# Kernel optimization log

Measured on AMD Instinct MI355X. Metric: run time of the kernel, lower is better.

Reference implementation:

```python
import jax, jax.numpy as jnp
import numpy as np

DIM_CAP = 16   # capsule dim
NCLS = 17      # annotation_nr
BS = 16
T = 120        # chunk_size * fps
P = 22         # players per frame graph
G = BS * T     # number of graphs = 1920
N = G * P      # nodes = 42240
C_IN = 14
CHS = [16, 32, 64, 152]  # 8m,16m,32m,76m with m=2
BN_EPS = 1e-3


def _build_graph():
    # fully-connected directed edges within each 22-node graph (no self loops)
    ii, jj = np.meshgrid(np.arange(P), np.arange(P), indexing='ij')
    mask = ii != jj
    li, lj = ii[mask], jj[mask]               # (462,)
    base = (np.arange(G) * P)[:, None]
    src = (base + li[None, :]).reshape(-1)
    dst = (base + lj[None, :]).reshape(-1)
    edge_index = np.stack([src, dst]).astype(np.int64)   # (2, E)
    batch = np.repeat(np.arange(G), P).astype(np.int64)  # (N,)
    return jnp.asarray(edge_index), jnp.asarray(batch)


def setup_inputs() -> dict:
    key = jax.random.key(0)
    ks = jax.random.split(key, 16)
    edge_index, batch = _build_graph()
    E = edge_index.shape[1]
    x = jax.random.normal(ks[0], (N, C_IN), dtype=jnp.float32)
    edge_attr = jax.random.uniform(ks[1], (E, 5), dtype=jnp.float32)
    dims = [C_IN] + CHS
    params = {}
    for i in range(4):
        s = 1.0 / np.sqrt(dims[i])
        params[f'W{i+1}'] = jax.random.normal(ks[2 + i], (dims[i], dims[i + 1]), dtype=jnp.float32) * s
        params[f'b{i+1}'] = jnp.zeros((dims[i + 1],), dtype=jnp.float32)
    c_out = DIM_CAP * NCLS  # 272
    params['conv_w'] = jax.random.normal(ks[6], (c_out, CHS[-1], 3), dtype=jnp.float32) * (1.0 / np.sqrt(CHS[-1] * 3))
    params['conv_b'] = jnp.zeros((c_out,), dtype=jnp.float32)
    params['bn_gamma'] = jnp.ones((T,), dtype=jnp.float32)
    params['bn_beta'] = jnp.zeros((T,), dtype=jnp.float32)
    return dict(x=x, edge_index=edge_index, batch=batch, edge_attr=edge_attr, **params)


def _gcn_layer(x, src, dst, w_edge, W, b):
    # PyG GCNConv: x' = D^-1/2 (A + I) D^-1/2 (x W) + b, edge weights w, self-loop weight 1
    n = x.shape[0]
    h = x @ W
    loop = jnp.arange(n)
    src_f = jnp.concatenate([src, loop])
    dst_f = jnp.concatenate([dst, loop])
    w_f = jnp.concatenate([w_edge, jnp.ones((n,), h.dtype)])
    deg = jax.ops.segment_sum(w_f, dst_f, num_segments=n)
    dinv = jnp.where(deg > 0, jax.lax.rsqrt(deg), 0.0)
    norm = dinv[src_f] * w_f * dinv[dst_f]
    out = jax.ops.segment_sum(norm[:, None] * h[src_f], dst_f, num_segments=n)
    return out + b


def reference(x, edge_index, batch, edge_attr, W1, b1, W2, b2, W3, b3, W4, b4,
              conv_w, conv_b, bn_gamma, bn_beta):
    src, dst = edge_index[0], edge_index[1]
    ew = edge_attr[:, 4]
    h = jax.nn.relu(_gcn_layer(x, src, dst, ew, W1, b1))
    h = jax.nn.relu(_gcn_layer(h, src, dst, ew, W2, b2))
    h = jax.nn.relu(_gcn_layer(h, src, dst, ew, W3, b3))
    h = jax.nn.relu(_gcn_layer(h, src, dst, ew, W4, b4))
    # global mean pool per graph -> (G, 152)
    ones = jnp.ones((h.shape[0],), h.dtype)
    cnt = jax.ops.segment_sum(ones, batch, num_segments=G)
    pooled = jax.ops.segment_sum(h, batch, num_segments=G) / jnp.clip(cnt, 1.0)[:, None]
    # (BS, T, 152) -> (BS, 152, T); conv kernel (3,1) with pad (1,1) on T
    feat = pooled.reshape(BS, T, CHS[-1]).transpose(0, 2, 1)
    conv = jax.lax.conv_general_dilated(
        feat, conv_w, window_strides=(1,), padding=[(1, 1)],
        dimension_numbers=('NCH', 'OIH', 'NCH'))
    conv = conv + conv_b[None, :, None]            # (BS, 272, T)
    caps = conv.transpose(0, 2, 1).reshape(BS, T, DIM_CAP, NCLS)
    # BatchNorm2d(num_features=T) in eval mode: running mean 0, var 1
    scale = (bn_gamma / jnp.sqrt(1.0 + BN_EPS))[None, :, None, None]
    shift = bn_beta[None, :, None, None]
    s = jax.nn.sigmoid(caps * scale + shift)
    out = jnp.sqrt(jnp.sum(jnp.square(s - 0.5), axis=2) * 4.0 / DIM_CAP)
    return out  # (BS, T, NCLS)
```

## Files before the change

kernel.cpp:

```cpp
#include <hip/hip_runtime.h>

#define GROUPS 1920

__device__ __forceinline__ int rh(int r) { return (r + (r >> 3)) & 7; }
__device__ __forceinline__ int swz(int r, int c) {
    return (r << 5) + ((((c >> 2) ^ rh(r)) << 2) | (c & 3));
}
__device__ __forceinline__ int swz4(int r, int c4) {
    return (r << 5) + ((c4 ^ rh(r)) << 2);
}

template<int DIN, int KR>
__device__ __forceinline__ void layerA(const float* buf, float* Ut,
                                       const float* A, int tid)
{
    constexpr int NT = (DIN / KR) * 3;
    if (tid < NT) {
        const int kt = tid / 3, pt = tid - kt * 3;
        const int p0 = pt * 8;
        float acc[KR][8];
        #pragma unroll
        for (int j = 0; j < KR; ++j)
            #pragma unroll
            for (int a = 0; a < 8; ++a) acc[j][a] = 0.f;
        #pragma unroll 2
        for (int q = 0; q < 22; ++q) {
            const float4 a0 = *(const float4*)(A + q * 28 + p0);
            const float4 a1 = *(const float4*)(A + q * 28 + p0 + 4);
            float xv[KR];
            #pragma unroll
            for (int j = 0; j < KR; ++j) xv[j] = buf[swz(kt * KR + j, q)];
            #pragma unroll
            for (int j = 0; j < KR; ++j) {
                acc[j][0] = fmaf(xv[j], a0.x, acc[j][0]);
                acc[j][1] = fmaf(xv[j], a0.y, acc[j][1]);
                acc[j][2] = fmaf(xv[j], a0.z, acc[j][2]);
                acc[j][3] = fmaf(xv[j], a0.w, acc[j][3]);
                acc[j][4] = fmaf(xv[j], a1.x, acc[j][4]);
                acc[j][5] = fmaf(xv[j], a1.y, acc[j][5]);
                acc[j][6] = fmaf(xv[j], a1.z, acc[j][6]);
                acc[j][7] = fmaf(xv[j], a1.w, acc[j][7]);
            }
        }
        #pragma unroll
        for (int j = 0; j < KR; ++j) {
            const int k = kt * KR + j;
            *(float4*)(Ut + swz4(k, pt * 2)) =
                make_float4(acc[j][0], acc[j][1], acc[j][2], acc[j][3]);
            *(float4*)(Ut + swz4(k, pt * 2 + 1)) =
                make_float4(acc[j][4], acc[j][5], acc[j][6], acc[j][7]);
        }
    }
}

template<int DIN, int DOUT, int CR>
__device__ __forceinline__ void layerB(const float* __restrict__ W,
                                       const float* __restrict__ Bb,
                                       const float* Ut, float* buf, int tid)
{
    constexpr int NT = (DOUT / CR) * 3;
    if (tid < NT) {
        const int ct = tid / 3, pt = tid - ct * 3;
        const int c0 = ct * CR;
        float acc[CR][8];
        #pragma unroll
        for (int b = 0; b < CR; ++b) {
            const float bias = Bb[c0 + b];
            #pragma unroll
            for (int a = 0; a < 8; ++a) acc[b][a] = bias;
        }
        #pragma unroll 4
        for (int k = 0; k < DIN; ++k) {
            const float4 u0 = *(const float4*)(Ut + swz4(k, pt * 2));
            const float4 u1 = *(const float4*)(Ut + swz4(k, pt * 2 + 1));
            float wv[CR];
            if constexpr (CR == 1) {
                wv[0] = W[k * DOUT + c0];
            } else if constexpr (CR == 2) {
                const float2 w2 = *(const float2*)(W + k * DOUT + c0);
                wv[0] = w2.x; wv[1] = w2.y;
            } else {
                #pragma unroll
                for (int b = 0; b < CR; b += 4) {
                    const float4 w4 = *(const float4*)(W + k * DOUT + c0 + b);
                    wv[b] = w4.x; wv[b + 1] = w4.y; wv[b + 2] = w4.z; wv[b + 3] = w4.w;
                }
            }
            #pragma unroll
            for (int b = 0; b < CR; ++b) {
                acc[b][0] = fmaf(wv[b], u0.x, acc[b][0]);
                acc[b][1] = fmaf(wv[b], u0.y, acc[b][1]);
                acc[b][2] = fmaf(wv[b], u0.z, acc[b][2]);
                acc[b][3] = fmaf(wv[b], u0.w, acc[b][3]);
                acc[b][4] = fmaf(wv[b], u1.x, acc[b][4]);
                acc[b][5] = fmaf(wv[b], u1.y, acc[b][5]);
                acc[b][6] = fmaf(wv[b], u1.z, acc[b][6]);
                acc[b][7] = fmaf(wv[b], u1.w, acc[b][7]);
            }
        }
        #pragma unroll
        for (int b = 0; b < CR; ++b) {
            const int r = c0 + b;
            *(float4*)(buf + swz4(r, pt * 2)) =
                make_float4(fmaxf(acc[b][0], 0.f), fmaxf(acc[b][1], 0.f),
                            fmaxf(acc[b][2], 0.f), fmaxf(acc[b][3], 0.f));
            *(float4*)(buf + swz4(r, pt * 2 + 1)) =
                make_float4(fmaxf(acc[b][4], 0.f), fmaxf(acc[b][5], 0.f),
                            fmaxf(acc[b][6], 0.f), fmaxf(acc[b][7], 0.f));
        }
    }
}

__global__ __launch_bounds__(128, 4) void gcn_kernel(
    const float* __restrict__ x, const float* __restrict__ ea,
    const float* __restrict__ W1, const float* __restrict__ b1,
    const float* __restrict__ W2, const float* __restrict__ b2,
    const float* __restrict__ W3, const float* __restrict__ b3,
    const float* __restrict__ W4, const float* __restrict__ b4,
    float* __restrict__ pT)
{
    __shared__ __align__(16) float sA[24 * 28];
    __shared__ float dv[24];
    __shared__ __align__(16) float buf[64 * 32];
    __shared__ __align__(16) float Ut[64 * 32];

    const int tid = threadIdx.x;
    const int g = blockIdx.x;
    const int b = g / 120, t = g - b * 120;

    if (t == 0)
        for (int j = tid; j < 152 * 4; j += 128)
            pT[(((size_t)(b * 152) + (j >> 2)) << 7) + (j & 3)] = 0.f;
    if (t == 119)
        for (int j = tid; j < 152 * 4; j += 128)
            pT[(((size_t)(b * 152) + (j >> 2)) << 7) + 124 + (j & 3)] = 0.f;

    for (int idx = tid; idx < 24 * 28; idx += 128) {
        const int q = idx / 28, p = idx - q * 28;
        float v = 0.f;
        if (q < 22 && p < 22) {
            if (q == p) v = 1.0f;
            else {
                const int e = q * 21 + p - (p > q);
                v = ea[((size_t)g * 462 + e) * 5 + 4];
            }
        }
        sA[idx] = v;
    }
    for (int idx = tid; idx < 14 * 24; idx += 128) {
        const int k = idx / 24, p = idx - k * 24;
        buf[swz(k, p)] = (p < 22) ? x[((size_t)g * 22 + p) * 14 + k] : 0.f;
    }
    __syncthreads();

    if (tid < 24) {
        const int p = tid;
        float s = 0.f;
        #pragma unroll
        for (int q = 0; q < 22; ++q) s += sA[q * 28 + p];
        dv[p] = (s > 0.f) ? rsqrtf(s) : 0.f;
    }
    __syncthreads();
    for (int idx = tid; idx < 24 * 28; idx += 128) {
        const int q = idx / 28, p = idx - q * 28;
        if (p < 24) sA[idx] *= dv[q] * dv[p];
    }
    __syncthreads();

    layerA<14, 1>(buf, Ut, sA, tid);           __syncthreads();
    layerB<14, 16, 1>(W1, b1, Ut, buf, tid);   __syncthreads();
    layerA<16, 1>(buf, Ut, sA, tid);           __syncthreads();
    layerB<16, 32, 2>(W2, b2, Ut, buf, tid);   __syncthreads();
    layerA<32, 2>(buf, Ut, sA, tid);           __syncthreads();
    layerB<32, 64, 4>(W3, b3, Ut, buf, tid);   __syncthreads();
    layerA<64, 4>(buf, Ut, sA, tid);           __syncthreads();

    float* pscr = sA;
    if (tid < 19 * 3) {
        const int ct = tid / 3, pt = tid - ct * 3;
        const int c0 = ct * 8;
        float acc[8][8];
        #pragma unroll
        for (int bb = 0; bb < 8; ++bb) {
            const float bias = b4[c0 + bb];
            #pragma unroll
            for (int a = 0; a < 8; ++a) acc[bb][a] = bias;
        }
        #pragma unroll 2
        for (int k = 0; k < 64; ++k) {
            const float4 u0 = *(const float4*)(Ut + swz4(k, pt * 2));
            const float4 u1 = *(const float4*)(Ut + swz4(k, pt * 2 + 1));
            const float4 wa = *(const float4*)(W4 + k * 152 + c0);
            const float4 wb = *(const float4*)(W4 + k * 152 + c0 + 4);
            const float wv[8] = {wa.x, wa.y, wa.z, wa.w, wb.x, wb.y, wb.z, wb.w};
            #pragma unroll
            for (int bb = 0; bb < 8; ++bb) {
                acc[bb][0] = fmaf(wv[bb], u0.x, acc[bb][0]);
                acc[bb][1] = fmaf(wv[bb], u0.y, acc[bb][1]);
                acc[bb][2] = fmaf(wv[bb], u0.z, acc[bb][2]);
                acc[bb][3] = fmaf(wv[bb], u0.w, acc[bb][3]);
                acc[bb][4] = fmaf(wv[bb], u1.x, acc[bb][4]);
                acc[bb][5] = fmaf(wv[bb], u1.y, acc[bb][5]);
                acc[bb][6] = fmaf(wv[bb], u1.z, acc[bb][6]);
                acc[bb][7] = fmaf(wv[bb], u1.w, acc[bb][7]);
            }
        }
        const int alim = (pt == 2) ? 6 : 8;
        float ps[8];
        #pragma unroll
        for (int bb = 0; bb < 8; ++bb) {
            float s = 0.f;
            #pragma unroll
            for (int a = 0; a < 8; ++a)
                s += (a < alim) ? fmaxf(acc[bb][a], 0.f) : 0.f;
            ps[bb] = s;
        }
        *(float4*)(pscr + pt * 152 + c0)     = make_float4(ps[0], ps[1], ps[2], ps[3]);
        *(float4*)(pscr + pt * 152 + c0 + 4) = make_float4(ps[4], ps[5], ps[6], ps[7]);
    }
    __syncthreads();

    {
        float* basep = pT + (((size_t)(b * 152)) << 7) + 4 + t;
        for (int c = tid; c < 152; c += 128) {
            const float s = pscr[c] + pscr[152 + c] + pscr[304 + c];
            basep[(size_t)c << 7] = s * (1.0f / 22.0f);
        }
    }
}

__global__ __launch_bounds__(512) void conv_caps_kernel(
    const float* __restrict__ pT, const float* __restrict__ cw,
    const float* __restrict__ cb, const float* __restrict__ gamma,
    const float* __restrict__ beta, float* __restrict__ out)
{
    __shared__ float sp[8 * 4 * 64];

    const int bx = blockIdx.x;
    const int b = bx / 34, r = bx - b * 34;
    const int n = r >> 1, thalf = r & 1;
    const int tid = threadIdx.x;
    const int w8 = __builtin_amdgcn_readfirstlane(tid >> 6);
    const int dq = w8 >> 1, ih = w8 & 1;
    const int lane = tid & 63;
    const bool act = (lane < 60);
    const int tt = act ? (thalf * 60 + lane) : 119;

    const int o0 = dq * 68 + n;
    float a0 = ih ? 0.f : cb[o0];
    float a1 = ih ? 0.f : cb[o0 + 17];
    float a2 = ih ? 0.f : cb[o0 + 34];
    float a3 = ih ? 0.f : cb[o0 + 51];

    const float* pf  = pT + (((size_t)(b * 152 + ih * 76)) << 7) + 3 + tt;
    const float* wp0 = cw + (size_t)o0 * 456 + ih * 228;
    const float* wp1 = wp0 + 17 * 456;
    const float* wp2 = wp0 + 34 * 456;
    const float* wp3 = wp0 + 51 * 456;

    for (int ib = 0; ib < 19; ++ib) {
        const int iw = ib * 12;
        float wv0[12], wv1[12], wv2[12], wv3[12];
        #pragma unroll
        for (int v = 0; v < 12; ++v) {
            wv0[v] = wp0[iw + v];
            wv1[v] = wp1[iw + v];
            wv2[v] = wp2[iw + v];
            wv3[v] = wp3[iw + v];
        }
        float fv[4][3];
        #pragma unroll
        for (int v = 0; v < 4; ++v) {
            const float* fi = pf + (((size_t)(ib * 4 + v)) << 7);
            fv[v][0] = fi[0]; fv[v][1] = fi[1]; fv[v][2] = fi[2];
        }
        #pragma unroll
        for (int v = 0; v < 4; ++v) {
            const float f0 = fv[v][0], f1 = fv[v][1], f2 = fv[v][2];
            a0 = fmaf(wv0[v*3], f0, fmaf(wv0[v*3+1], f1, fmaf(wv0[v*3+2], f2, a0)));
            a1 = fmaf(wv1[v*3], f0, fmaf(wv1[v*3+1], f1, fmaf(wv1[v*3+2], f2, a1)));
            a2 = fmaf(wv2[v*3], f0, fmaf(wv2[v*3+1], f1, fmaf(wv2[v*3+2], f2, a2)));
            a3 = fmaf(wv3[v*3], f0, fmaf(wv3[v*3+1], f1, fmaf(wv3[v*3+2], f2, a3)));
        }
    }

    sp[(w8 * 4 + 0) * 64 + lane] = a0;
    sp[(w8 * 4 + 1) * 64 + lane] = a1;
    sp[(w8 * 4 + 2) * 64 + lane] = a2;
    sp[(w8 * 4 + 3) * 64 + lane] = a3;
    __syncthreads();

    if (tid < 64) {
        const int ln = tid;
        const bool a2c = (ln < 60);
        const int t2 = a2c ? (thalf * 60 + ln) : 119;
        const float sct = gamma[t2] * 0.999500374688f;
        const float sht = beta[t2];
        float ss = 0.f;
        #pragma unroll
        for (int q2 = 0; q2 < 4; ++q2) {
            #pragma unroll
            for (int j = 0; j < 4; ++j) {
                const float v = sp[((q2 * 2 + 0) * 4 + j) * 64 + ln]
                              + sp[((q2 * 2 + 1) * 4 + j) * 64 + ln];
                const float z = fmaf(v, sct, sht);
                const float s = 1.0f / (1.0f + __expf(-z));
                const float d = s - 0.5f;
                ss += d * d;
            }
        }
        if (a2c) out[((size_t)b * 120 + t2) * 17 + n] = sqrtf(ss) * 0.5f;
    }
}

extern "C" void kernel_launch(void* const* d_in, const int* in_sizes, int n_in,
                              void* d_out, int out_size, void* d_ws, size_t ws_size,
                              hipStream_t stream) {
    const float* x     = (const float*)d_in[0];
    const float* ea    = (const float*)d_in[3];
    const float* W1    = (const float*)d_in[4];
    const float* b1    = (const float*)d_in[5];
    const float* W2    = (const float*)d_in[6];
    const float* b2    = (const float*)d_in[7];
    const float* W3    = (const float*)d_in[8];
    const float* b3    = (const float*)d_in[9];
    const float* W4    = (const float*)d_in[10];
    const float* b4    = (const float*)d_in[11];
    const float* cw    = (const float*)d_in[12];
    const float* cb    = (const float*)d_in[13];
    const float* gamma = (const float*)d_in[14];
    const float* beta  = (const float*)d_in[15];
    float* out = (float*)d_out;

    float* pT = (float*)d_ws;

    hipLaunchKernelGGL(gcn_kernel, dim3(GROUPS), dim3(128), 0, stream,
                       x, ea, W1, b1, W2, b2, W3, b3, W4, b4, pT);
    hipLaunchKernelGGL(conv_caps_kernel, dim3(16 * 34), dim3(512), 0, stream,
                       pT, cw, cb, gamma, beta, out);
}
```

Before: 148.1 us.

## Split GCN node columns across two waves with wave-local LDS fences

Work is now split across both 64-lane waves by node-column tiles: each wave owns 3 of 6 four-column tiles, halving per-thread accumulators and using both waves where previously only the first ~57-96 threads were active. Because each wave computes Ut only for its own columns, the layerA to layerB barrier is replaced by a wave-local lgkmcnt wait. Ping-pong activation buffers (bufA/bufB) avoid write-after-read hazards across the remaining fewer block barriers. This costs extra LDS and a six-way final pooled sum.

```diff
diff --git a/kernel.cpp b/kernel.cpp
--- a/kernel.cpp
+++ b/kernel.cpp
@@ -1,6 +1,8 @@
 #include <hip/hip_runtime.h>
 
 #define GROUPS 1920
+
+#define WAVE_LDS_FENCE() asm volatile("s_waitcnt lgkmcnt(0)" ::: "memory")
 
 __device__ __forceinline__ int rh(int r) { return (r + (r >> 3)) & 7; }
 __device__ __forceinline__ int swz(int r, int c) {
@@ -11,68 +13,60 @@
 }
 
 template<int DIN, int KR>
-__device__ __forceinline__ void layerA(const float* buf, float* Ut,
-                                       const float* A, int tid)
+__device__ __forceinline__ void layerA2w(const float* bufIn, float* Ut,
+                                         const float* A, int w, int l)
 {
-    constexpr int NT = (DIN / KR) * 3;
-    if (tid < NT) {
-        const int kt = tid / 3, pt = tid - kt * 3;
-        const int p0 = pt * 8;
-        float acc[KR][8];
+    constexpr int NL = (DIN / KR) * 3;
+    if (l < NL) {
+        const int kt = l / 3;
+        const int pt = w * 3 + (l - kt * 3);
+        float acc[KR][4];
         #pragma unroll
         for (int j = 0; j < KR; ++j)
             #pragma unroll
-            for (int a = 0; a < 8; ++a) acc[j][a] = 0.f;
+            for (int a = 0; a < 4; ++a) acc[j][a] = 0.f;
         #pragma unroll 2
         for (int q = 0; q < 22; ++q) {
-            const float4 a0 = *(const float4*)(A + q * 28 + p0);
-            const float4 a1 = *(const float4*)(A + q * 28 + p0 + 4);
+            const float4 a0 = *(const float4*)(A + q * 28 + pt * 4);
             float xv[KR];
             #pragma unroll
-            for (int j = 0; j < KR; ++j) xv[j] = buf[swz(kt * KR + j, q)];
+            for (int j = 0; j < KR; ++j) xv[j] = bufIn[swz(kt * KR + j, q)];
             #pragma unroll
             for (int j = 0; j < KR; ++j) {
                 acc[j][0] = fmaf(xv[j], a0.x, acc[j][0]);
                 acc[j][1] = fmaf(xv[j], a0.y, acc[j][1]);
                 acc[j][2] = fmaf(xv[j], a0.z, acc[j][2]);
                 acc[j][3] = fmaf(xv[j], a0.w, acc[j][3]);
-                acc[j][4] = fmaf(xv[j], a1.x, acc[j][4]);
-                acc[j][5] = fmaf(xv[j], a1.y, acc[j][5]);
-                acc[j][6] = fmaf(xv[j], a1.z, acc[j][6]);
-                acc[j][7] = fmaf(xv[j], a1.w, acc[j][7]);
-            }
-        }
-        #pragma unroll
-        for (int j = 0; j < KR; ++j) {
-            const int k = kt * KR + j;
-            *(float4*)(Ut + swz4(k, pt * 2)) =
+            }
+        }
+        #pragma unroll
+        for (int j = 0; j < KR; ++j)
+            *(float4*)(Ut + swz4(kt * KR + j, pt)) =
                 make_float4(acc[j][0], acc[j][1], acc[j][2], acc[j][3]);
-            *(float4*)(Ut + swz4(k, pt * 2 + 1)) =
-                make_float4(acc[j][4], acc[j][5], acc[j][6], acc[j][7]);
-        }
     }
 }
 
 template<int DIN, int DOUT, int CR>
-__device__ __forceinline__ void layerB(const float* __restrict__ W,
-                                       const float* __restrict__ Bb,
-                                       const float* Ut, float* buf, int tid)
+__device__ __forceinline__ void layerB2w(const float* __restrict__ W,
+                                         const float* __restrict__ Bb,
+                                         const float* Ut, float* bufOut,
+                                         int w, int l)
 {
-    constexpr int NT = (DOUT / CR) * 3;
-    if (tid < NT) {
-        const int ct = tid / 3, pt = tid - ct * 3;
+    constexpr int NL = (DOUT / CR) * 3;
+    if (l < NL) {
+        const int ct = l / 3;
+        const int pt = w * 3 + (l - ct * 3);
         const int c0 = ct * CR;
-        float acc[CR][8];
+        float acc[CR][4];
         #pragma unroll
         for (int b = 0; b < CR; ++b) {
             const float bias = Bb[c0 + b];
             #pragma unroll
-            for (int a = 0; a < 8; ++a) acc[b][a] = bias;
+            for (int a = 0; a < 4; ++a) acc[b][a] = bias;
         }
         #pragma unroll 4
         for (int k = 0; k < DIN; ++k) {
-            const float4 u0 = *(const float4*)(Ut + swz4(k, pt * 2));
-            const float4 u1 = *(const float4*)(Ut + swz4(k, pt * 2 + 1));
+            const float4 u0 = *(const float4*)(Ut + swz4(k, pt));
             float wv[CR];
             if constexpr (CR == 1) {
                 wv[0] = W[k * DOUT + c0];
@@ -92,22 +86,13 @@
                 acc[b][1] = fmaf(wv[b], u0.y, acc[b][1]);
                 acc[b][2] = fmaf(wv[b], u0.z, acc[b][2]);
                 acc[b][3] = fmaf(wv[b], u0.w, acc[b][3]);
-                acc[b][4] = fmaf(wv[b], u1.x, acc[b][4]);
-                acc[b][5] = fmaf(wv[b], u1.y, acc[b][5]);
-                acc[b][6] = fmaf(wv[b], u1.z, acc[b][6]);
-                acc[b][7] = fmaf(wv[b], u1.w, acc[b][7]);
-            }
-        }
-        #pragma unroll
-        for (int b = 0; b < CR; ++b) {
-            const int r = c0 + b;
-            *(float4*)(buf + swz4(r, pt * 2)) =
+            }
+        }
+        #pragma unroll
+        for (int b = 0; b < CR; ++b)
+            *(float4*)(bufOut + swz4(c0 + b, pt)) =
                 make_float4(fmaxf(acc[b][0], 0.f), fmaxf(acc[b][1], 0.f),
                             fmaxf(acc[b][2], 0.f), fmaxf(acc[b][3], 0.f));
-            *(float4*)(buf + swz4(r, pt * 2 + 1)) =
-                make_float4(fmaxf(acc[b][4], 0.f), fmaxf(acc[b][5], 0.f),
-                            fmaxf(acc[b][6], 0.f), fmaxf(acc[b][7], 0.f));
-        }
     }
 }
 
@@ -121,12 +106,14 @@
 {
     __shared__ __align__(16) float sA[24 * 28];
     __shared__ float dv[24];
-    __shared__ __align__(16) float buf[64 * 32];
+    __shared__ __align__(16) float bufA[32 * 32];
+    __shared__ __align__(16) float bufB[64 * 32];
     __shared__ __align__(16) float Ut[64 * 32];
 
     const int tid = threadIdx.x;
     const int g = blockIdx.x;
     const int b = g / 120, t = g - b * 120;
+    const int w = tid >> 6, l = tid & 63;
 
     if (t == 0)
         for (int j = tid; j < 152 * 4; j += 128)
@@ -149,7 +136,7 @@
     }
     for (int idx = tid; idx < 14 * 24; idx += 128) {
         const int k = idx / 24, p = idx - k * 24;
-        buf[swz(k, p)] = (p < 22) ? x[((size_t)g * 22 + p) * 14 + k] : 0.f;
+        bufA[swz(k, p)] = (p < 22) ? x[((size_t)g * 22 + p) * 14 + k] : 0.f;
     }
     __syncthreads();
 
@@ -167,29 +154,29 @@
     }
     __syncthreads();
 
-    layerA<14, 1>(buf, Ut, sA, tid);           __syncthreads();
-    layerB<14, 16, 1>(W1, b1, Ut, buf, tid);   __syncthreads();
-    layerA<16, 1>(buf, Ut, sA, tid);           __syncthreads();
-    layerB<16, 32, 2>(W2, b2, Ut, buf, tid);   __syncthreads();
-    layerA<32, 2>(buf, Ut, sA, tid);           __syncthreads();
-    layerB<32, 64, 4>(W3, b3, Ut, buf, tid);   __syncthreads();
-    layerA<64, 4>(buf, Ut, sA, tid);           __syncthreads();
-
-    float* pscr = sA;
-    if (tid < 19 * 3) {
-        const int ct = tid / 3, pt = tid - ct * 3;
+    layerA2w<14, 1>(bufA, Ut, sA, w, l);          WAVE_LDS_FENCE();
+    layerB2w<14, 16, 1>(W1, b1, Ut, bufB, w, l);  __syncthreads();
+    layerA2w<16, 1>(bufB, Ut, sA, w, l);          WAVE_LDS_FENCE();
+    layerB2w<16, 32, 2>(W2, b2, Ut, bufA, w, l);  __syncthreads();
+    layerA2w<32, 2>(bufA, Ut, sA, w, l);          WAVE_LDS_FENCE();
+    layerB2w<32, 64, 4>(W3, b3, Ut, bufB, w, l);  __syncthreads();
+    layerA2w<64, 4>(bufB, Ut, sA, w, l);          WAVE_LDS_FENCE();
+
+    float* pscr = bufA;
+    if (l < 19 * 3) {
+        const int ct = l / 3;
+        const int pt = w * 3 + (l - ct * 3);
         const int c0 = ct * 8;
-        float acc[8][8];
+        float acc[8][4];
         #pragma unroll
         for (int bb = 0; bb < 8; ++bb) {
             const float bias = b4[c0 + bb];
             #pragma unroll
-            for (int a = 0; a < 8; ++a) acc[bb][a] = bias;
+            for (int a = 0; a < 4; ++a) acc[bb][a] = bias;
         }
         #pragma unroll 2
         for (int k = 0; k < 64; ++k) {
-            const float4 u0 = *(const float4*)(Ut + swz4(k, pt * 2));
-            const float4 u1 = *(const float4*)(Ut + swz4(k, pt * 2 + 1));
+            const float4 u0 = *(const float4*)(Ut + swz4(k, pt));
             const float4 wa = *(const float4*)(W4 + k * 152 + c0);
             const float4 wb = *(const float4*)(W4 + k * 152 + c0 + 4);
             const float wv[8] = {wa.x, wa.y, wa.z, wa.w, wb.x, wb.y, wb.z, wb.w};
@@ -199,19 +186,15 @@
                 acc[bb][1] = fmaf(wv[bb], u0.y, acc[bb][1]);
                 acc[bb][2] = fmaf(wv[bb], u0.z, acc[bb][2]);
                 acc[bb][3] = fmaf(wv[bb], u0.w, acc[bb][3]);
-                acc[bb][4] = fmaf(wv[bb], u1.x, acc[bb][4]);
-                acc[bb][5] = fmaf(wv[bb], u1.y, acc[bb][5]);
-                acc[bb][6] = fmaf(wv[bb], u1.z, acc[bb][6]);
-                acc[bb][7] = fmaf(wv[bb], u1.w, acc[bb][7]);
-            }
-        }
-        const int alim = (pt == 2) ? 6 : 8;
+            }
+        }
+        const int alim = (pt == 5) ? 2 : 4;
         float ps[8];
         #pragma unroll
         for (int bb = 0; bb < 8; ++bb) {
             float s = 0.f;
             #pragma unroll
-            for (int a = 0; a < 8; ++a)
+            for (int a = 0; a < 4; ++a)
                 s += (a < alim) ? fmaxf(acc[bb][a], 0.f) : 0.f;
             ps[bb] = s;
         }
@@ -223,7 +206,8 @@
     {
         float* basep = pT + (((size_t)(b * 152)) << 7) + 4 + t;
         for (int c = tid; c < 152; c += 128) {
-            const float s = pscr[c] + pscr[152 + c] + pscr[304 + c];
+            const float s = ((((pscr[c] + pscr[152 + c]) + pscr[304 + c])
+                            + pscr[456 + c]) + pscr[608 + c]) + pscr[760 + c];
             basep[(size_t)c << 7] = s * (1.0f / 22.0f);
         }
     }
```

Measured after the change: 165.5 us. 1.12x slower.
